# Optimization experiments

Measured on AMD Instinct MI355X. Metric: run time of the kernel, lower is better.

The kernel has to match this reference:

```python
import jax, jax.numpy as jnp
import numpy as np

EMB_DIM = 1024
D_K = 64
B, S = 4, 4096

def setup_inputs() -> dict:
    key = jax.random.key(0)
    ks = jax.random.split(key, 8)
    inv = 1.0 / np.sqrt(EMB_DIM)
    return {
        "input1": jax.random.normal(ks[0], (B, S, EMB_DIM), dtype=jnp.float32),
        "input2": jax.random.normal(ks[1], (B, S, EMB_DIM), dtype=jnp.float32),
        "Wq": jax.random.uniform(ks[2], (EMB_DIM, D_K), jnp.float32, -inv, inv),
        "bq": jax.random.uniform(ks[3], (D_K,), jnp.float32, -inv, inv),
        "Wk": jax.random.uniform(ks[4], (EMB_DIM, D_K), jnp.float32, -inv, inv),
        "bk": jax.random.uniform(ks[5], (D_K,), jnp.float32, -inv, inv),
        "Wv": jax.random.uniform(ks[6], (EMB_DIM, D_K), jnp.float32, -inv, inv),
        "bv": jax.random.uniform(ks[7], (D_K,), jnp.float32, -inv, inv),
    }

def reference(input1, input2, Wq, bq, Wk, bk, Wv, bv):
    # queries from input2; keys/values from input1 (as in the torch forward)
    q = input2 @ Wq + bq            # [B, Sq, d_k]
    k = input1 @ Wk + bk            # [B, Sk, d_k]
    v = input1 @ Wv + bv            # [B, Sk, d_k]
    scale = 1.0 / jnp.sqrt(jnp.asarray(D_K, q.dtype))
    scores = jnp.einsum("bqd,bkd->bqk", q, k) * scale  # [B, Sq, Sk]
    attn = jax.nn.softmax(scores, axis=-1)
    return jnp.einsum("bqk,bkd->bqd", attn, v)          # [B, Sq, d_k]
```

## Files before the change

### kernel.cpp

```cpp
#include <hip/hip_runtime.h>
#include <hip/hip_bf16.h>

#define E 1024
#define DK 64
#define SEQ 4096
#define NB 4
#define NSPLIT 4
#define KSCALE 0.125f

typedef short bf16x8 __attribute__((ext_vector_type(8)));
typedef short bf16x4 __attribute__((ext_vector_type(4)));
typedef float f32x4 __attribute__((ext_vector_type(4)));

__device__ inline unsigned short f2bf(float f) {
    unsigned int u = __float_as_uint(f);
    u += 0x7fff + ((u >> 16) & 1);
    return (unsigned short)(u >> 16);
}
__device__ inline unsigned int pkbf(float a, float b) {
    return (unsigned int)f2bf(a) | ((unsigned int)f2bf(b) << 16);
}

__global__ __launch_bounds__(256) void wt_kernel(
    const float* __restrict__ Wq, const float* __restrict__ Wk, const float* __restrict__ Wv,
    unsigned short* __restrict__ wtq, unsigned short* __restrict__ wtk, unsigned short* __restrict__ wtv)
{
    const float* src; unsigned short* dst;
    if (blockIdx.y == 0)      { src = Wq; dst = wtq; }
    else if (blockIdx.y == 1) { src = Wk; dst = wtk; }
    else                      { src = Wv; dst = wtv; }
    const int tid = threadIdx.x;
    const int e0 = blockIdx.x * 64;
    __shared__ float Ws[64][65];
    #pragma unroll
    for (int i = 0; i < 4; ++i) {
        int flat = i * 256 + tid;
        int r = flat >> 4;
        int c4 = (flat & 15) << 2;
        float4 v = *reinterpret_cast<const float4*>(&src[(size_t)(e0 + r) * DK + c4]);
        Ws[c4 + 0][r] = v.x; Ws[c4 + 1][r] = v.y; Ws[c4 + 2][r] = v.z; Ws[c4 + 3][r] = v.w;
    }
    __syncthreads();
    #pragma unroll
    for (int i = 0; i < 4; ++i) {
        int flat = i * 256 + tid;
        int c = flat >> 4;
        int r4 = (flat & 15) << 2;
        ushort4 o;
        o.x = f2bf(Ws[c][r4 + 0]); o.y = f2bf(Ws[c][r4 + 1]);
        o.z = f2bf(Ws[c][r4 + 2]); o.w = f2bf(Ws[c][r4 + 3]);
        *reinterpret_cast<ushort4*>(&dst[(size_t)c * E + e0 + r4]) = o;
    }
}

#define APAD 88
#define WPAD 80
__global__ __launch_bounds__(256, 2) void proj_kernel(
    const float* __restrict__ in_q, const float* __restrict__ in_kv,
    const unsigned short* __restrict__ wtq, const unsigned short* __restrict__ wtk,
    const unsigned short* __restrict__ wtv,
    const float* __restrict__ bq, const float* __restrict__ bk, const float* __restrict__ bv,
    unsigned short* __restrict__ Qw, unsigned short* __restrict__ Kw, unsigned short* __restrict__ Vtw)
{
    const int tid = threadIdx.x;
    const int w = tid >> 6, lane = tid & 63, quad = lane >> 4, l16 = lane & 15;
    const int row0 = blockIdx.x * 64;
    const bool isQ = (blockIdx.y == 0);
    const float* A = isQ ? in_q : in_kv;
    const unsigned short* w0 = isQ ? wtq : wtk;

    __shared__ unsigned short As[2][64][APAD];
    __shared__ unsigned short Ws0[2][64][WPAD];
    __shared__ unsigned short Ws1[2][64][WPAD];

    const int arow = tid >> 4, acol = (tid & 15) << 2;
    const int wrow = tid >> 3, wch = (tid & 7) << 3;

    {
        #pragma unroll
        for (int i = 0; i < 4; ++i) {
            int flat = i * 256 + tid;
            int r = flat >> 4, c4 = (flat & 15) << 2;
            float4 v = *reinterpret_cast<const float4*>(&A[(size_t)(row0 + r) * E + c4]);
            unsigned int lo = pkbf(v.x, v.y), hi = pkbf(v.z, v.w);
            *reinterpret_cast<uint2*>(&As[0][r][c4]) = make_uint2(lo, hi);
        }
        #pragma unroll
        for (int i = 0; i < 2; ++i) {
            int r = i * 32 + wrow;
            *reinterpret_cast<uint4*>(&Ws0[0][r][wch]) =
                *reinterpret_cast<const uint4*>(&w0[(size_t)r * E + wch]);
            if (!isQ)
                *reinterpret_cast<uint4*>(&Ws1[0][r][wch]) =
                    *reinterpret_cast<const uint4*>(&wtv[(size_t)r * E + wch]);
        }
    }
    __syncthreads();

    f32x4 acc0[4] = {};
    f32x4 acc1[4] = {};

    for (int kb = 0; kb < 16; ++kb) {
        const int cur = kb & 1, nxt = cur ^ 1;
        const bool pf = (kb < 15);
        float4 av[4];
        uint4 wv0[2], wv1[2];
        if (pf) {
            const int ko = (kb + 1) * 64;
            #pragma unroll
            for (int i = 0; i < 4; ++i) {
                int flat = i * 256 + tid;
                int r = flat >> 4, c4 = (flat & 15) << 2;
                av[i] = *reinterpret_cast<const float4*>(&A[(size_t)(row0 + r) * E + ko + c4]);
            }
            #pragma unroll
            for (int i = 0; i < 2; ++i) {
                int r = i * 32 + wrow;
                wv0[i] = *reinterpret_cast<const uint4*>(&w0[(size_t)r * E + ko + wch]);
                if (!isQ)
                    wv1[i] = *reinterpret_cast<const uint4*>(&wtv[(size_t)r * E + ko + wch]);
            }
        }
        #pragma unroll
        for (int ks = 0; ks < 2; ++ks) {
            bf16x8 af = *reinterpret_cast<const bf16x8*>(&As[cur][w * 16 + l16][ks * 32 + quad * 8]);
            #pragma unroll
            for (int ct = 0; ct < 4; ++ct) {
                bf16x8 b0 = *reinterpret_cast<const bf16x8*>(&Ws0[cur][ct * 16 + l16][ks * 32 + quad * 8]);
                acc0[ct] = __builtin_amdgcn_mfma_f32_16x16x32_bf16(af, b0, acc0[ct], 0, 0, 0);
                if (!isQ) {
                    bf16x8 b1 = *reinterpret_cast<const bf16x8*>(&Ws1[cur][ct * 16 + l16][ks * 32 + quad * 8]);
                    acc1[ct] = __builtin_amdgcn_mfma_f32_16x16x32_bf16(af, b1, acc1[ct], 0, 0, 0);
                }
            }
        }
        if (pf) {
            #pragma unroll
            for (int i = 0; i < 4; ++i) {
                int flat = i * 256 + tid;
                int r = flat >> 4, c4 = (flat & 15) << 2;
                unsigned int lo = pkbf(av[i].x, av[i].y), hi = pkbf(av[i].z, av[i].w);
                *reinterpret_cast<uint2*>(&As[nxt][r][c4]) = make_uint2(lo, hi);
            }
            #pragma unroll
            for (int i = 0; i < 2; ++i) {
                int r = i * 32 + wrow;
                *reinterpret_cast<uint4*>(&Ws0[nxt][r][wch]) = wv0[i];
                if (!isQ) *reinterpret_cast<uint4*>(&Ws1[nxt][r][wch]) = wv1[i];
            }
            __syncthreads();
        }
    }

    const int orow0 = row0 + w * 16 + quad * 4;
    #pragma unroll
    for (int ct = 0; ct < 4; ++ct) {
        int col = ct * 16 + l16;
        if (isQ) {
            float bias = bq[col];
            #pragma unroll
            for (int r = 0; r < 4; ++r)
                Qw[(size_t)(orow0 + r) * DK + col] = f2bf(acc0[ct][r] + bias);
        } else {
            float biask = bk[col], biasv = bv[col];
            #pragma unroll
            for (int r = 0; r < 4; ++r) {
                int grow = orow0 + r;
                Kw[(size_t)grow * DK + col] = f2bf((acc0[ct][r] + biask) * KSCALE);
                int bb = grow >> 12;
                int tok = grow & 4095;
                Vtw[((size_t)(bb * 64 + col)) * SEQ + tok] = f2bf(acc1[ct][r] + biasv);
            }
        }
    }
}

#define KPAD 88
__global__ __launch_bounds__(256, 2) void attn_kernel(
    const unsigned short* __restrict__ Qw, const unsigned short* __restrict__ Kw,
    const unsigned short* __restrict__ Vtw, float* __restrict__ Opart, float* __restrict__ lpart)
{
    const int tid = threadIdx.x;
    const int w = tid >> 6, lane = tid & 63, quad = lane >> 4, l16 = lane & 15;
    const int x = blockIdx.x;
    const int s = x & 3;
    const int qt = (x >> 2) & 63;
    const int b = x >> 8;

    __shared__ unsigned short Ks[2][64][KPAD];
    __shared__ unsigned short Vts[2][64][KPAD];
    __shared__ float LDSf[4][16][66];
    __shared__ float LDSl[4][4][16];

    bf16x8 qfb[2][4];
    #pragma unroll
    for (int ks = 0; ks < 2; ++ks)
        #pragma unroll
        for (int ct = 0; ct < 4; ++ct)
            qfb[ks][ct] = *reinterpret_cast<const bf16x8*>(
                &Qw[((size_t)(b * SEQ + qt * 64 + ct * 16 + l16)) * DK + ks * 32 + quad * 8]);

    const int kt0 = s * 16;
    const int srow = (tid & 255) >> 3;

    {
        const int gk = kt0 * 64;
        #pragma unroll
        for (int i = 0; i < 2; ++i) {
            int flat = i * 256 + tid;
            int r = flat >> 3, ch = (flat & 7) << 3;
            *reinterpret_cast<uint4*>(&Ks[0][r][ch]) =
                *reinterpret_cast<const uint4*>(&Kw[((size_t)(b * SEQ + gk + r)) * DK + ch]);
            *reinterpret_cast<uint4*>(&Vts[0][r][ch]) =
                *reinterpret_cast<const uint4*>(&Vtw[((size_t)(b * 64 + r)) * SEQ + gk + ch]);
        }
    }
    __syncthreads();

    float lp[4] = {0.f, 0.f, 0.f, 0.f};
    f32x4 o[4][4] = {};

    for (int kt = 0; kt < 16; ++kt) {
        const int cur = kt & 1, nxt = cur ^ 1;
        const bool pf = (kt < 15);
        uint4 stk[2], stv[2];
        int r0 = 0, r1 = 0, ch0 = 0, ch1 = 0;
        if (pf) {
            const int gk = (kt0 + kt + 1) * 64;
            #pragma unroll
            for (int i = 0; i < 2; ++i) {
                int flat = i * 256 + tid;
                int r = flat >> 3, ch = (flat & 7) << 3;
                if (i == 0) { r0 = r; ch0 = ch; } else { r1 = r; ch1 = ch; }
                stk[i] = *reinterpret_cast<const uint4*>(&Kw[((size_t)(b * SEQ + gk + r)) * DK + ch]);
                stv[i] = *reinterpret_cast<const uint4*>(&Vtw[((size_t)(b * 64 + r)) * SEQ + gk + ch]);
            }
        }

        bf16x8 kf0 = *reinterpret_cast<const bf16x8*>(&Ks[cur][w * 16 + l16][quad * 8]);
        bf16x8 kf1 = *reinterpret_cast<const bf16x8*>(&Ks[cur][w * 16 + l16][32 + quad * 8]);

        f32x4 sacc[4] = {};
        #pragma unroll
        for (int ct = 0; ct < 4; ++ct) {
            sacc[ct] = __builtin_amdgcn_mfma_f32_16x16x32_bf16(kf0, qfb[0][ct], sacc[ct], 0, 0, 0);
            sacc[ct] = __builtin_amdgcn_mfma_f32_16x16x32_bf16(kf1, qfb[1][ct], sacc[ct], 0, 0, 0);
        }

        bf16x4 va[4];
        #pragma unroll
        for (int ct = 0; ct < 4; ++ct)
            va[ct] = *reinterpret_cast<const bf16x4*>(&Vts[cur][ct * 16 + l16][w * 16 + quad * 4]);

        #pragma unroll
        for (int cq = 0; cq < 4; ++cq) {
            float p0 = __expf(sacc[cq][0]);
            float p1 = __expf(sacc[cq][1]);
            float p2 = __expf(sacc[cq][2]);
            float p3 = __expf(sacc[cq][3]);
            lp[cq] += (p0 + p1) + (p2 + p3);
            bf16x4 pb = { (short)f2bf(p0), (short)f2bf(p1), (short)f2bf(p2), (short)f2bf(p3) };
            #pragma unroll
            for (int cd = 0; cd < 4; ++cd)
                o[cd][cq] = __builtin_amdgcn_mfma_f32_16x16x16bf16_1k(va[cd], pb, o[cd][cq], 0, 0, 0);
        }

        if (pf) {
            *reinterpret_cast<uint4*>(&Ks[nxt][r0][ch0]) = stk[0];
            *reinterpret_cast<uint4*>(&Ks[nxt][r1][ch1]) = stk[1];
            *reinterpret_cast<uint4*>(&Vts[nxt][r0][ch0]) = stv[0];
            *reinterpret_cast<uint4*>(&Vts[nxt][r1][ch1]) = stv[1];
            __syncthreads();
        }
    }
    (void)srow;

    #pragma unroll
    for (int cq = 0; cq < 4; ++cq) {
        float t = lp[cq];
        t += __shfl_xor(t, 16, 64);
        t += __shfl_xor(t, 32, 64);
        lp[cq] = t;
    }
    if (lane < 16)
        #pragma unroll
        for (int cq = 0; cq < 4; ++cq)
            LDSl[w][cq][lane] = lp[cq];

    const int ql = tid >> 4, d4 = (tid & 15) << 2;
    #pragma unroll
    for (int cq = 0; cq < 4; ++cq) {
        #pragma unroll
        for (int cd = 0; cd < 4; ++cd)
            *reinterpret_cast<f32x4*>(&LDSf[w][l16][cd * 16 + quad * 4]) = o[cd][cq];
        __syncthreads();
        f32x4 acc = {};
        #pragma unroll
        for (int w2 = 0; w2 < 4; ++w2)
            acc += *reinterpret_cast<const f32x4*>(&LDSf[w2][ql][d4]);
        *reinterpret_cast<f32x4*>(
            &Opart[(size_t)s * (NB * SEQ * DK)
                   + ((size_t)(b * SEQ + qt * 64 + cq * 16 + ql)) * DK + d4]) = acc;
        if ((tid & 15) == 0) {
            float lq = LDSl[0][cq][ql] + LDSl[1][cq][ql] + LDSl[2][cq][ql] + LDSl[3][cq][ql];
            lpart[(size_t)s * (NB * SEQ) + b * SEQ + qt * 64 + cq * 16 + ql] = lq;
        }
        __syncthreads();
    }
}

__global__ __launch_bounds__(256) void combine_kernel(
    const float* __restrict__ Opart, const float* __restrict__ lpart, float* __restrict__ out)
{
    const int idx = blockIdx.x * 256 + threadIdx.x;
    const int base = idx << 2;
    const int row = base >> 6;
    f32x4 acc = {};
    float lt = 0.f;
    #pragma unroll
    for (int s = 0; s < NSPLIT; ++s) {
        f32x4 v = *reinterpret_cast<const f32x4*>(&Opart[(size_t)s * (NB * SEQ * DK) + base]);
        acc += v;
        lt += lpart[(size_t)s * (NB * SEQ) + row];
    }
    float inv = 1.f / lt;
    *reinterpret_cast<f32x4*>(&out[base]) = acc * inv;
}

extern "C" void kernel_launch(void* const* d_in, const int* in_sizes, int n_in,
                              void* d_out, int out_size, void* d_ws, size_t ws_size,
                              hipStream_t stream) {
    const float* input1 = (const float*)d_in[0];
    const float* input2 = (const float*)d_in[1];
    const float* Wq = (const float*)d_in[2];
    const float* bq = (const float*)d_in[3];
    const float* Wk = (const float*)d_in[4];
    const float* bk = (const float*)d_in[5];
    const float* Wv = (const float*)d_in[6];
    const float* bv = (const float*)d_in[7];
    float* out = (float*)d_out;

    char* ws = (char*)d_ws;
    unsigned short* wtq = (unsigned short*)(ws + 0);
    unsigned short* wtk = (unsigned short*)(ws + 131072);
    unsigned short* wtv = (unsigned short*)(ws + 262144);
    unsigned short* Qw  = (unsigned short*)(ws + 393216);
    unsigned short* Kw  = (unsigned short*)(ws + 2490368);
    unsigned short* Vtw = (unsigned short*)(ws + 4587520);
    float* Opart        = (float*)(ws + 6684672);
    float* lpart        = (float*)(ws + 6684672 + 16777216);

    wt_kernel<<<dim3(16, 3), 256, 0, stream>>>(Wq, Wk, Wv, wtq, wtk, wtv);
    proj_kernel<<<dim3(256, 2), 256, 0, stream>>>(input2, input1, wtq, wtk, wtv,
                                                  bq, bk, bv, Qw, Kw, Vtw);
    attn_kernel<<<dim3(1024), 256, 0, stream>>>(Qw, Kw, Vtw, Opart, lpart);
    combine_kernel<<<dim3(1024), 256, 0, stream>>>(Opart, lpart, out);
}
```

Measured before the change: 234.9 us.

## Use direct global-to-LDS loads with XOR swizzle and drop split-K combine pass

Projection and attention kernels now stage tiles with global_load_lds straight into LDS, using an XOR-swizzled unpadded layout for bf16 tiles. The projection keeps fp32 activations in LDS and converts to bf16 on read. Attention no longer splits the key range four ways, so the Opart/lpart workspace and the combine kernel go away and normalization happens in place. The cost is fewer blocks (256 instead of 1024), which can underfill the GPU's compute units, and each block now runs a longer serial loop over keys.

```diff
diff --git a/kernel.cpp b/kernel.cpp
--- a/kernel.cpp
+++ b/kernel.cpp
@@ -5,20 +5,20 @@
 #define DK 64
 #define SEQ 4096
 #define NB 4
-#define NSPLIT 4
 #define KSCALE 0.125f
+#define AROW 68
 
 typedef short bf16x8 __attribute__((ext_vector_type(8)));
 typedef short bf16x4 __attribute__((ext_vector_type(4)));
 typedef float f32x4 __attribute__((ext_vector_type(4)));
+
+typedef const __attribute__((address_space(1))) unsigned int* gcp;
+typedef __attribute__((address_space(3))) unsigned int* lcp;
 
 __device__ inline unsigned short f2bf(float f) {
     unsigned int u = __float_as_uint(f);
     u += 0x7fff + ((u >> 16) & 1);
     return (unsigned short)(u >> 16);
-}
-__device__ inline unsigned int pkbf(float a, float b) {
-    return (unsigned int)f2bf(a) | ((unsigned int)f2bf(b) << 16);
 }
 
 __global__ __launch_bounds__(256) void wt_kernel(
@@ -53,8 +53,6 @@
     }
 }
 
-#define APAD 88
-#define WPAD 80
 __global__ __launch_bounds__(256, 2) void proj_kernel(
     const float* __restrict__ in_q, const float* __restrict__ in_kv,
     const unsigned short* __restrict__ wtq, const unsigned short* __restrict__ wtk,
@@ -69,30 +67,29 @@
     const float* A = isQ ? in_q : in_kv;
     const unsigned short* w0 = isQ ? wtq : wtk;
 
-    __shared__ unsigned short As[2][64][APAD];
-    __shared__ unsigned short Ws0[2][64][WPAD];
-    __shared__ unsigned short Ws1[2][64][WPAD];
-
-    const int arow = tid >> 4, acol = (tid & 15) << 2;
-    const int wrow = tid >> 3, wch = (tid & 7) << 3;
+    __shared__ float As[2][64 * AROW];
+    __shared__ unsigned short W0s[2][64 * 64];
+    __shared__ unsigned short W1s[2][64 * 64];
+
+    const int rl = lane >> 3, pp = lane & 7;
 
     {
         #pragma unroll
-        for (int i = 0; i < 4; ++i) {
-            int flat = i * 256 + tid;
-            int r = flat >> 4, c4 = (flat & 15) << 2;
-            float4 v = *reinterpret_cast<const float4*>(&A[(size_t)(row0 + r) * E + c4]);
-            unsigned int lo = pkbf(v.x, v.y), hi = pkbf(v.z, v.w);
-            *reinterpret_cast<uint2*>(&As[0][r][c4]) = make_uint2(lo, hi);
+        for (int i = 0; i < 16; ++i) {
+            int r = w * 16 + i;
+            const float* src = A + (size_t)(row0 + r) * E + lane;
+            __builtin_amdgcn_global_load_lds((gcp)(const void*)src, (lcp)(void*)&As[0][r * AROW], 4, 0, 0);
         }
         #pragma unroll
         for (int i = 0; i < 2; ++i) {
-            int r = i * 32 + wrow;
-            *reinterpret_cast<uint4*>(&Ws0[0][r][wch]) =
-                *reinterpret_cast<const uint4*>(&w0[(size_t)r * E + wch]);
+            int g = w * 2 + i;
+            int r = g * 8 + rl;
+            int lc = pp ^ (r & 7);
+            __builtin_amdgcn_global_load_lds((gcp)(const void*)(w0 + (size_t)r * E + lc * 8),
+                                             (lcp)(void*)&W0s[0][g * 512], 16, 0, 0);
             if (!isQ)
-                *reinterpret_cast<uint4*>(&Ws1[0][r][wch]) =
-                    *reinterpret_cast<const uint4*>(&wtv[(size_t)r * E + wch]);
+                __builtin_amdgcn_global_load_lds((gcp)(const void*)(wtv + (size_t)r * E + lc * 8),
+                                                 (lcp)(void*)&W1s[0][g * 512], 16, 0, 0);
         }
     }
     __syncthreads();
@@ -100,56 +97,51 @@
     f32x4 acc0[4] = {};
     f32x4 acc1[4] = {};
 
+    #pragma unroll 2
     for (int kb = 0; kb < 16; ++kb) {
         const int cur = kb & 1, nxt = cur ^ 1;
         const bool pf = (kb < 15);
-        float4 av[4];
-        uint4 wv0[2], wv1[2];
         if (pf) {
             const int ko = (kb + 1) * 64;
             #pragma unroll
-            for (int i = 0; i < 4; ++i) {
-                int flat = i * 256 + tid;
-                int r = flat >> 4, c4 = (flat & 15) << 2;
-                av[i] = *reinterpret_cast<const float4*>(&A[(size_t)(row0 + r) * E + ko + c4]);
+            for (int i = 0; i < 16; ++i) {
+                int r = w * 16 + i;
+                const float* src = A + (size_t)(row0 + r) * E + ko + lane;
+                __builtin_amdgcn_global_load_lds((gcp)(const void*)src, (lcp)(void*)&As[nxt][r * AROW], 4, 0, 0);
             }
             #pragma unroll
             for (int i = 0; i < 2; ++i) {
-                int r = i * 32 + wrow;
-                wv0[i] = *reinterpret_cast<const uint4*>(&w0[(size_t)r * E + ko + wch]);
+                int g = w * 2 + i;
+                int r = g * 8 + rl;
+                int lc = pp ^ (r & 7);
+                __builtin_amdgcn_global_load_lds((gcp)(const void*)(w0 + (size_t)r * E + ko + lc * 8),
+                                                 (lcp)(void*)&W0s[nxt][g * 512], 16, 0, 0);
                 if (!isQ)
-                    wv1[i] = *reinterpret_cast<const uint4*>(&wtv[(size_t)r * E + ko + wch]);
-            }
-        }
+                    __builtin_amdgcn_global_load_lds((gcp)(const void*)(wtv + (size_t)r * E + ko + lc * 8),
+                                                     (lcp)(void*)&W1s[nxt][g * 512], 16, 0, 0);
+            }
+        }
+        const int arow = w * 16 + l16;
         #pragma unroll
         for (int ks = 0; ks < 2; ++ks) {
-            bf16x8 af = *reinterpret_cast<const bf16x8*>(&As[cur][w * 16 + l16][ks * 32 + quad * 8]);
+            const float* ap = &As[cur][arow * AROW + ks * 32 + quad * 8];
+            f32x4 a0 = *reinterpret_cast<const f32x4*>(ap);
+            f32x4 a1 = *reinterpret_cast<const f32x4*>(ap + 4);
+            bf16x8 af = { (short)f2bf(a0[0]), (short)f2bf(a0[1]), (short)f2bf(a0[2]), (short)f2bf(a0[3]),
+                          (short)f2bf(a1[0]), (short)f2bf(a1[1]), (short)f2bf(a1[2]), (short)f2bf(a1[3]) };
             #pragma unroll
             for (int ct = 0; ct < 4; ++ct) {
-                bf16x8 b0 = *reinterpret_cast<const bf16x8*>(&Ws0[cur][ct * 16 + l16][ks * 32 + quad * 8]);
+                int brow = ct * 16 + l16;
+                int pc = (ks * 4 + quad) ^ (brow & 7);
+                bf16x8 b0 = *reinterpret_cast<const bf16x8*>(&W0s[cur][brow * 64 + pc * 8]);
                 acc0[ct] = __builtin_amdgcn_mfma_f32_16x16x32_bf16(af, b0, acc0[ct], 0, 0, 0);
                 if (!isQ) {
-                    bf16x8 b1 = *reinterpret_cast<const bf16x8*>(&Ws1[cur][ct * 16 + l16][ks * 32 + quad * 8]);
+                    bf16x8 b1 = *reinterpret_cast<const bf16x8*>(&W1s[cur][brow * 64 + pc * 8]);
                     acc1[ct] = __builtin_amdgcn_mfma_f32_16x16x32_bf16(af, b1, acc1[ct], 0, 0, 0);
                 }
             }
         }
-        if (pf) {
-            #pragma unroll
-            for (int i = 0; i < 4; ++i) {
-                int flat = i * 256 + tid;
-                int r = flat >> 4, c4 = (flat & 15) << 2;
-                unsigned int lo = pkbf(av[i].x, av[i].y), hi = pkbf(av[i].z, av[i].w);
-                *reinterpret_cast<uint2*>(&As[nxt][r][c4]) = make_uint2(lo, hi);
-            }
-            #pragma unroll
-            for (int i = 0; i < 2; ++i) {
-                int r = i * 32 + wrow;
-                *reinterpret_cast<uint4*>(&Ws0[nxt][r][wch]) = wv0[i];
-                if (!isQ) *reinterpret_cast<uint4*>(&Ws1[nxt][r][wch]) = wv1[i];
-            }
-            __syncthreads();
-        }
+        if (pf) __syncthreads();
     }
 
     const int orow0 = row0 + w * 16 + quad * 4;
@@ -175,21 +167,18 @@
     }
 }
 
-#define KPAD 88
-__global__ __launch_bounds__(256, 2) void attn_kernel(
+__global__ __launch_bounds__(256) void attn_kernel(
     const unsigned short* __restrict__ Qw, const unsigned short* __restrict__ Kw,
-    const unsigned short* __restrict__ Vtw, float* __restrict__ Opart, float* __restrict__ lpart)
+    const unsigned short* __restrict__ Vtw, float* __restrict__ out)
 {
     const int tid = threadIdx.x;
     const int w = tid >> 6, lane = tid & 63, quad = lane >> 4, l16 = lane & 15;
-    const int x = blockIdx.x;
-    const int s = x & 3;
-    const int qt = (x >> 2) & 63;
-    const int b = x >> 8;
-
-    __shared__ unsigned short Ks[2][64][KPAD];
-    __shared__ unsigned short Vts[2][64][KPAD];
-    __shared__ float LDSf[4][16][66];
+    const int qt = blockIdx.x & 63;
+    const int b = blockIdx.x >> 6;
+
+    __shared__ unsigned short Ks[2][64 * 64];
+    __shared__ unsigned short Vts[2][64 * 64];
+    __shared__ float LDSf[4][16][68];
     __shared__ float LDSl[4][4][16];
 
     bf16x8 qfb[2][4];
@@ -200,45 +189,44 @@
             qfb[ks][ct] = *reinterpret_cast<const bf16x8*>(
                 &Qw[((size_t)(b * SEQ + qt * 64 + ct * 16 + l16)) * DK + ks * 32 + quad * 8]);
 
-    const int kt0 = s * 16;
-    const int srow = (tid & 255) >> 3;
-
-    {
-        const int gk = kt0 * 64;
-        #pragma unroll
-        for (int i = 0; i < 2; ++i) {
-            int flat = i * 256 + tid;
-            int r = flat >> 3, ch = (flat & 7) << 3;
-            *reinterpret_cast<uint4*>(&Ks[0][r][ch]) =
-                *reinterpret_cast<const uint4*>(&Kw[((size_t)(b * SEQ + gk + r)) * DK + ch]);
-            *reinterpret_cast<uint4*>(&Vts[0][r][ch]) =
-                *reinterpret_cast<const uint4*>(&Vtw[((size_t)(b * 64 + r)) * SEQ + gk + ch]);
-        }
+    const int rl = lane >> 3, pp = lane & 7;
+
+    #pragma unroll
+    for (int i = 0; i < 2; ++i) {
+        int g = w * 2 + i;
+        int r = g * 8 + rl;
+        int lc = pp ^ (r & 7);
+        __builtin_amdgcn_global_load_lds((gcp)(const void*)&Kw[((size_t)(b * SEQ + r)) * DK + lc * 8],
+                                         (lcp)(void*)&Ks[0][g * 512], 16, 0, 0);
+        __builtin_amdgcn_global_load_lds((gcp)(const void*)&Vtw[((size_t)(b * 64 + r)) * SEQ + lc * 8],
+                                         (lcp)(void*)&Vts[0][g * 512], 16, 0, 0);
     }
     __syncthreads();
 
     float lp[4] = {0.f, 0.f, 0.f, 0.f};
     f32x4 o[4][4] = {};
 
-    for (int kt = 0; kt < 16; ++kt) {
+    #pragma unroll 2
+    for (int kt = 0; kt < 64; ++kt) {
         const int cur = kt & 1, nxt = cur ^ 1;
-        const bool pf = (kt < 15);
-        uint4 stk[2], stv[2];
-        int r0 = 0, r1 = 0, ch0 = 0, ch1 = 0;
+        const bool pf = (kt < 63);
         if (pf) {
-            const int gk = (kt0 + kt + 1) * 64;
+            const int gk = (kt + 1) * 64;
             #pragma unroll
             for (int i = 0; i < 2; ++i) {
-                int flat = i * 256 + tid;
-                int r = flat >> 3, ch = (flat & 7) << 3;
-                if (i == 0) { r0 = r; ch0 = ch; } else { r1 = r; ch1 = ch; }
-                stk[i] = *reinterpret_cast<const uint4*>(&Kw[((size_t)(b * SEQ + gk + r)) * DK + ch]);
-                stv[i] = *reinterpret_cast<const uint4*>(&Vtw[((size_t)(b * 64 + r)) * SEQ + gk + ch]);
-            }
-        }
-
-        bf16x8 kf0 = *reinterpret_cast<const bf16x8*>(&Ks[cur][w * 16 + l16][quad * 8]);
-        bf16x8 kf1 = *reinterpret_cast<const bf16x8*>(&Ks[cur][w * 16 + l16][32 + quad * 8]);
+                int g = w * 2 + i;
+                int r = g * 8 + rl;
+                int lc = pp ^ (r & 7);
+                __builtin_amdgcn_global_load_lds((gcp)(const void*)&Kw[((size_t)(b * SEQ + gk + r)) * DK + lc * 8],
+                                                 (lcp)(void*)&Ks[nxt][g * 512], 16, 0, 0);
+                __builtin_amdgcn_global_load_lds((gcp)(const void*)&Vtw[((size_t)(b * 64 + r)) * SEQ + gk + lc * 8],
+                                                 (lcp)(void*)&Vts[nxt][g * 512], 16, 0, 0);
+            }
+        }
+
+        const int krow = w * 16 + l16;
+        bf16x8 kf0 = *reinterpret_cast<const bf16x8*>(&Ks[cur][krow * 64 + ((quad) ^ (krow & 7)) * 8]);
+        bf16x8 kf1 = *reinterpret_cast<const bf16x8*>(&Ks[cur][krow * 64 + ((4 + quad) ^ (krow & 7)) * 8]);
 
         f32x4 sacc[4] = {};
         #pragma unroll
@@ -249,8 +237,11 @@
 
         bf16x4 va[4];
         #pragma unroll
-        for (int ct = 0; ct < 4; ++ct)
-            va[ct] = *reinterpret_cast<const bf16x4*>(&Vts[cur][ct * 16 + l16][w * 16 + quad * 4]);
+        for (int ct = 0; ct < 4; ++ct) {
+            int vrow = ct * 16 + l16;
+            int pc = (w * 2 + (quad >> 1)) ^ (vrow & 7);
+            va[ct] = *reinterpret_cast<const bf16x4*>(&Vts[cur][vrow * 64 + pc * 8 + (quad & 1) * 4]);
+        }
 
         #pragma unroll
         for (int cq = 0; cq < 4; ++cq) {
@@ -265,15 +256,8 @@
                 o[cd][cq] = __builtin_amdgcn_mfma_f32_16x16x16bf16_1k(va[cd], pb, o[cd][cq], 0, 0, 0);
         }
 
-        if (pf) {
-            *reinterpret_cast<uint4*>(&Ks[nxt][r0][ch0]) = stk[0];
-            *reinterpret_cast<uint4*>(&Ks[nxt][r1][ch1]) = stk[1];
-            *reinterpret_cast<uint4*>(&Vts[nxt][r0][ch0]) = stv[0];
-            *reinterpret_cast<uint4*>(&Vts[nxt][r1][ch1]) = stv[1];
-            __syncthreads();
-        }
-    }
-    (void)srow;
+        if (pf) __syncthreads();
+    }
 
     #pragma unroll
     for (int cq = 0; cq < 4; ++cq) {
@@ -298,33 +282,11 @@
         #pragma unroll
         for (int w2 = 0; w2 < 4; ++w2)
             acc += *reinterpret_cast<const f32x4*>(&LDSf[w2][ql][d4]);
-        *reinterpret_cast<f32x4*>(
-            &Opart[(size_t)s * (NB * SEQ * DK)
-                   + ((size_t)(b * SEQ + qt * 64 + cq * 16 + ql)) * DK + d4]) = acc;
-        if ((tid & 15) == 0) {
-            float lq = LDSl[0][cq][ql] + LDSl[1][cq][ql] + LDSl[2][cq][ql] + LDSl[3][cq][ql];
-            lpart[(size_t)s * (NB * SEQ) + b * SEQ + qt * 64 + cq * 16 + ql] = lq;
-        }
+        float lq = LDSl[0][cq][ql] + LDSl[1][cq][ql] + LDSl[2][cq][ql] + LDSl[3][cq][ql];
+        f32x4 res = acc * (1.0f / lq);
+        *reinterpret_cast<f32x4*>(&out[((size_t)(b * SEQ + qt * 64 + cq * 16 + ql)) * DK + d4]) = res;
         __syncthreads();
     }
-}
-
-__global__ __launch_bounds__(256) void combine_kernel(
-    const float* __restrict__ Opart, const float* __restrict__ lpart, float* __restrict__ out)
-{
-    const int idx = blockIdx.x * 256 + threadIdx.x;
-    const int base = idx << 2;
-    const int row = base >> 6;
-    f32x4 acc = {};
-    float lt = 0.f;
-    #pragma unroll
-    for (int s = 0; s < NSPLIT; ++s) {
-        f32x4 v = *reinterpret_cast<const f32x4*>(&Opart[(size_t)s * (NB * SEQ * DK) + base]);
-        acc += v;
-        lt += lpart[(size_t)s * (NB * SEQ) + row];
-    }
-    float inv = 1.f / lt;
-    *reinterpret_cast<f32x4*>(&out[base]) = acc * inv;
 }
 
 extern "C" void kernel_launch(void* const* d_in, const int* in_sizes, int n_in,
@@ -347,12 +309,9 @@
     unsigned short* Qw  = (unsigned short*)(ws + 393216);
     unsigned short* Kw  = (unsigned short*)(ws + 2490368);
     unsigned short* Vtw = (unsigned short*)(ws + 4587520);
-    float* Opart        = (float*)(ws + 6684672);
-    float* lpart        = (float*)(ws + 6684672 + 16777216);
 
     wt_kernel<<<dim3(16, 3), 256, 0, stream>>>(Wq, Wk, Wv, wtq, wtk, wtv);
     proj_kernel<<<dim3(256, 2), 256, 0, stream>>>(input2, input1, wtq, wtk, wtv,
                                                   bq, bk, bv, Qw, Kw, Vtw);
-    attn_kernel<<<dim3(1024), 256, 0, stream>>>(Qw, Kw, Vtw, Opart, lpart);
-    combine_kernel<<<dim3(1024), 256, 0, stream>>>(Opart, lpart, out);
-}
+    attn_kernel<<<dim3(256), 256, 0, stream>>>(Qw, Kw, Vtw, out);
+}
```

New measurement: 229.2 us. 2.4% less time.
